# Kernel tuning notes

Measured on AMD Instinct MI355X. Metric: run time of the kernel, lower is better.

## Reference

```python
import jax, jax.numpy as jnp
import numpy as np

K = 32   # tokens_per_obs (hard-coded in module)
V = 512  # vocab_size

def setup_inputs() -> dict:
    key = jax.random.key(0)
    ks = jax.random.split(key, 10)
    s = 0.02  # small init scale for numerical sanity
    return {
        "x": jax.random.normal(ks[0], (4096, 512), jnp.float32),
        "enc_w1": jax.random.normal(ks[1], (512, 512), jnp.float32) * s,
        "enc_b1": jnp.zeros((512,), jnp.float32),
        "enc_w2": jax.random.normal(ks[2], (512, 16384), jnp.float32) * s,
        "enc_b2": jnp.zeros((16384,), jnp.float32),
        "codebook": jax.random.uniform(ks[3], (16384, 256), jnp.float32, -1.0 / V, 1.0 / V),
        "dec_w1": jax.random.normal(ks[4], (256, 512), jnp.float32) * s,
        "dec_b1": jnp.zeros((512,), jnp.float32),
        "dec_w2": jax.random.normal(ks[5], (512, 512), jnp.float32) * s,
        "dec_b2": jnp.zeros((512,), jnp.float32),
    }

def reference(x, enc_w1, enc_b1, enc_w2, enc_b2, codebook,
              dec_w1, dec_b1, dec_w2, dec_b2):
    b = x.shape[0]
    # encoder MLP -> logits z of shape (b, K*V)
    h = jax.nn.relu(x @ enc_w1 + enc_b1)
    z = h @ enc_w2 + enc_b2
    zl = z.reshape(b, K, V)                      # (b, K, V) per-block logits
    # categorical sample per token block
    tokens = jax.random.categorical(jax.random.key(1), zl, axis=-1)  # (b, K) int
    p = jax.nn.softmax(zl, axis=-1).reshape(b, K * V)
    oh = jax.nn.one_hot(tokens, V, dtype=p.dtype).reshape(b, K * V)
    # straight-through: forward value == one-hot, gradient flows through p
    st = p + jax.lax.stop_gradient(oh - p)
    z_q = st @ codebook                          # (b, embed_dim) = sum of K code rows
    # decoder MLP -> reconstruction
    rec = jax.nn.relu(z_q @ dec_w1 + dec_b1) @ dec_w2 + dec_b2
    return z, z_q, rec
```

## Files before the change

kernel.cpp:

```cpp
#include <hip/hip_runtime.h>
#include <hip/hip_bf16.h>
#include <math.h>
#include <stdint.h>


#define BATCH 4096
#define KTOK  32
#define VOCAB 512
#define DMODEL 512
#define ZDIM  16384
#define EDIM  256
#define MARGIN 0.03125f

typedef __attribute__((ext_vector_type(8))) short short8v;
typedef __attribute__((ext_vector_type(4))) float f32x4;

__device__ __forceinline__ void threefry2x32(uint32_t k0, uint32_t k1,
                                             uint32_t x0, uint32_t x1,
                                             uint32_t& y0, uint32_t& y1) {
    uint32_t ks0 = k0, ks1 = k1, ks2 = k0 ^ k1 ^ 0x1BD11BDAu;
    x0 += ks0; x1 += ks1;
#define TFR(r) { x0 += x1; x1 = __builtin_rotateleft32(x1, r); x1 ^= x0; }
    TFR(13) TFR(15) TFR(26) TFR(6)
    x0 += ks1; x1 += ks2 + 1u;
    TFR(17) TFR(29) TFR(16) TFR(24)
    x0 += ks2; x1 += ks0 + 2u;
    TFR(13) TFR(15) TFR(26) TFR(6)
    x0 += ks0; x1 += ks1 + 3u;
    TFR(17) TFR(29) TFR(16) TFR(24)
    x0 += ks1; x1 += ks2 + 4u;
    TFR(13) TFR(15) TFR(26) TFR(6)
    x0 += ks2; x1 += ks0 + 5u;
#undef TFR
    y0 = x0; y1 = x1;
}

__device__ __forceinline__ float jax_gumbel(uint64_t e) {
    const float TINY = 1.17549435e-38f;
    uint32_t y0, y1;
    threefry2x32(0u, 1u, (uint32_t)(e >> 32), (uint32_t)(e & 0xffffffffull), y0, y1);
    uint32_t bits = y0 ^ y1;
    float u = __uint_as_float(0x3f800000u | (bits >> 9)) - 1.0f;
    u = u * 1.0f + TINY;
    u = fmaxf(TINY, u);
    return -logf(-logf(u));
}

__device__ __forceinline__ float gumbel_from_bits(uint32_t bits) {
    const float TINY = 1.17549435e-38f;
    const float LN2 = 0.69314718056f;
    float f = __uint_as_float(0x3f800000u | (bits >> 9));
    float u = f - 1.0f;
    float d = 2.0f - f;
    u = fmaxf(u, TINY);
    float e_hw = -LN2 * __builtin_amdgcn_logf(u);
    float e_poly = d * fmaf(d, fmaf(d, 0.33333333f, 0.5f), 1.0f);
    float e = (d < 0.002f) ? e_poly : e_hw;
    return -LN2 * __builtin_amdgcn_logf(e);
}

__device__ __forceinline__ float fast_gumbel(uint32_t e32) {
    uint32_t y0, y1;
    threefry2x32(0u, 1u, 0u, e32, y0, y1);
    return gumbel_from_bits(y0 ^ y1);
}

__device__ __forceinline__ unsigned short f32_to_bf16_rne(float f) {
    uint32_t u = __float_as_uint(f);
    uint32_t r = (u + 0x7fffu + ((u >> 16) & 1u)) >> 16;
    return (unsigned short)r;
}

__device__ __forceinline__ void top2_push(float& s1, float& s2, int& v1,
                                          float s, int v) {
    if (s > s1 || (s == s1 && v < v1)) { s2 = s1; s1 = s; v1 = v; }
    else s2 = fmaxf(s2, s);
}
__device__ __forceinline__ void top2_merge(float& s1, float& s2, int& v1,
                                           float os1, float os2, int ov1) {
    if (os1 > s1 || (os1 == s1 && ov1 < v1)) {
        s2 = fmaxf(s1, os2);
        s1 = os1; v1 = ov1;
    } else {
        s2 = fmaxf(s2, os1);
    }
}

__device__ __forceinline__ void gload16(const unsigned short* src,
                                        unsigned short* lds_base) {
    __builtin_amdgcn_global_load_lds(
        (const __attribute__((address_space(1))) unsigned int*)src,
        (__attribute__((address_space(3))) unsigned int*)lds_base, 16, 0, 0);
}

template<bool RELU>
__global__ __launch_bounds__(256)
void gemm_f32_64(const float* __restrict__ A, const float* __restrict__ B,
                 const float* __restrict__ bias, float* __restrict__ C,
                 unsigned short* __restrict__ Cb,
                 int M, int N, int K) {
    constexpr int BK = 16;
    __shared__ __align__(16) float As[BK][68];
    __shared__ __align__(16) float Bs[BK][68];

    const int tid = threadIdx.x;
    const int tx = tid % 16;
    const int ty = tid / 16;
    const int brow = blockIdx.y * 64;
    const int bcol = blockIdx.x * 64;

    float acc[4][4] = {};

    for (int k0 = 0; k0 < K; k0 += BK) {
        {
            int r = tid >> 2, c4 = tid & 3;
            float4 v = *(const float4*)&A[(size_t)(brow + r) * K + k0 + c4 * 4];
            As[c4 * 4 + 0][r] = v.x;
            As[c4 * 4 + 1][r] = v.y;
            As[c4 * 4 + 2][r] = v.z;
            As[c4 * 4 + 3][r] = v.w;
        }
        {
            int r = tid >> 4, c4 = tid & 15;
            *(float4*)&Bs[r][c4 * 4] = *(const float4*)&B[(size_t)(k0 + r) * N + bcol + c4 * 4];
        }
        __syncthreads();

#pragma unroll
        for (int kk = 0; kk < BK; ++kk) {
            float a[4], b[4];
            *(float4*)&a[0] = *(const float4*)&As[kk][ty * 4];
            *(float4*)&b[0] = *(const float4*)&Bs[kk][tx * 4];
#pragma unroll
            for (int i = 0; i < 4; ++i)
#pragma unroll
                for (int j = 0; j < 4; ++j)
                    acc[i][j] = fmaf(a[i], b[j], acc[i][j]);
        }
        __syncthreads();
    }

#pragma unroll
    for (int i = 0; i < 4; ++i) {
        int row = brow + ty * 4 + i;
        int col = bcol + tx * 4;
        float4 v;
        v.x = acc[i][0] + bias[col + 0];
        v.y = acc[i][1] + bias[col + 1];
        v.z = acc[i][2] + bias[col + 2];
        v.w = acc[i][3] + bias[col + 3];
        if (RELU) {
            v.x = fmaxf(v.x, 0.0f); v.y = fmaxf(v.y, 0.0f);
            v.z = fmaxf(v.z, 0.0f); v.w = fmaxf(v.w, 0.0f);
        }
        *(float4*)&C[(size_t)row * N + col] = v;
        if (Cb) {
            ushort4 o;
            o.x = f32_to_bf16_rne(v.x);
            o.y = f32_to_bf16_rne(v.y);
            o.z = f32_to_bf16_rne(v.z);
            o.w = f32_to_bf16_rne(v.w);
            *(ushort4*)&Cb[(size_t)row * N + col] = o;
        }
    }
}

template<bool RELU>
__global__ __launch_bounds__(256)
void gemm_f32(const float* __restrict__ A, const float* __restrict__ B,
              const float* __restrict__ bias, float* __restrict__ C,
              int M, int N, int K) {
    constexpr int BM = 128, BN = 128, BK = 16, TM = 8, TN = 8;
    __shared__ __align__(16) float As[BK][BM + 4];
    __shared__ __align__(16) float Bs[BK][BN + 4];

    const int tid = threadIdx.x;
    const int tx = tid % (BN / TN);
    const int ty = tid / (BN / TN);
    const int brow = blockIdx.y * BM;
    const int bcol = blockIdx.x * BN;

    float acc[TM][TN] = {};

    for (int k0 = 0; k0 < K; k0 += BK) {
#pragma unroll
        for (int f = tid; f < BM * BK / 4; f += 256) {
            int r = f / (BK / 4);
            int c4 = f % (BK / 4);
            float4 v = *(const float4*)&A[(size_t)(brow + r) * K + k0 + c4 * 4];
            As[c4 * 4 + 0][r] = v.x;
            As[c4 * 4 + 1][r] = v.y;
            As[c4 * 4 + 2][r] = v.z;
            As[c4 * 4 + 3][r] = v.w;
        }
#pragma unroll
        for (int f = tid; f < BK * BN / 4; f += 256) {
            int r = f / (BN / 4);
            int c4 = f % (BN / 4);
            *(float4*)&Bs[r][c4 * 4] = *(const float4*)&B[(size_t)(k0 + r) * N + bcol + c4 * 4];
        }
        __syncthreads();

#pragma unroll
        for (int kk = 0; kk < BK; ++kk) {
            float a[TM], b[TN];
            *(float4*)&a[0] = *(const float4*)&As[kk][ty * TM];
            *(float4*)&a[4] = *(const float4*)&As[kk][ty * TM + 4];
            *(float4*)&b[0] = *(const float4*)&Bs[kk][tx * TN];
            *(float4*)&b[4] = *(const float4*)&Bs[kk][tx * TN + 4];
#pragma unroll
            for (int i = 0; i < TM; ++i)
#pragma unroll
                for (int j = 0; j < TN; ++j)
                    acc[i][j] = fmaf(a[i], b[j], acc[i][j]);
        }
        __syncthreads();
    }

#pragma unroll
    for (int i = 0; i < TM; ++i) {
        int row = brow + ty * TM + i;
#pragma unroll
        for (int j = 0; j < TN; j += 4) {
            int col = bcol + tx * TN + j;
            float4 v;
            v.x = acc[i][j + 0] + bias[col + 0];
            v.y = acc[i][j + 1] + bias[col + 1];
            v.z = acc[i][j + 2] + bias[col + 2];
            v.w = acc[i][j + 3] + bias[col + 3];
            if (RELU) {
                v.x = fmaxf(v.x, 0.0f); v.y = fmaxf(v.y, 0.0f);
                v.z = fmaxf(v.z, 0.0f); v.w = fmaxf(v.w, 0.0f);
            }
            *(float4*)&C[(size_t)row * N + col] = v;
        }
    }
}

__global__ __launch_bounds__(256)
void transpose_w2(const float* __restrict__ src, unsigned short* __restrict__ dstb,
                  float* __restrict__ dstf, int R, int C, int writeF) {
    __shared__ float tile[32][33];
    const int c0 = blockIdx.x * 32, r0 = blockIdx.y * 32;
    const int tx = threadIdx.x % 32, ty = threadIdx.x / 32;
#pragma unroll
    for (int i = ty; i < 32; i += 8)
        tile[i][tx] = src[(size_t)(r0 + i) * C + c0 + tx];
    __syncthreads();
#pragma unroll
    for (int i = ty; i < 32; i += 8) {
        float v = tile[tx][i];
        size_t o = (size_t)(c0 + i) * R + r0 + tx;
        dstb[o] = f32_to_bf16_rne(v);
        if (writeF) dstf[o] = v;
    }
}

__global__ __launch_bounds__(256)
void gemm_mfma_bf16(const unsigned short* __restrict__ A,
                    const unsigned short* __restrict__ Bt,
                    const float* __restrict__ bias,
                    float* __restrict__ C,
                    int M, int N, int K) {
    constexpr int BM = 128, BN = 128, BK = 32;
    __shared__ unsigned short As[BM * BK];
    __shared__ unsigned short Bs[BN * BK];

    const int lid = blockIdx.y * gridDim.x + blockIdx.x;
    const int xcd = lid & 7;
    const int kk2 = lid >> 3;
    const int rpx = gridDim.y >> 3;
    const int by = xcd * rpx + (kk2 % rpx);
    const int bx = kk2 / rpx;

    const int tid = threadIdx.x;
    const int wid = tid >> 6;
    const int lane = tid & 63;
    const int wr = wid >> 1, wc = wid & 1;
    const int l15 = lane & 15, lq = lane >> 4;
    const int brow = by * BM;
    const int bcol = bx * BN;

    const int g1 = tid;
    const int g2 = tid + 256;
    const size_t a1 = (size_t)(brow + (g1 >> 2)) * K + (g1 & 3) * 8;
    const size_t a2 = (size_t)(brow + (g2 >> 2)) * K + (g2 & 3) * 8;
    const size_t b1 = (size_t)(bcol + (g1 >> 2)) * K + (g1 & 3) * 8;
    const size_t b2 = (size_t)(bcol + (g2 >> 2)) * K + (g2 & 3) * 8;
    unsigned short* as_base1 = As + (size_t)wid * 64 * 8;
    unsigned short* as_base2 = As + (size_t)(256 + wid * 64) * 8;
    unsigned short* bs_base1 = Bs + (size_t)wid * 64 * 8;
    unsigned short* bs_base2 = Bs + (size_t)(256 + wid * 64) * 8;

    f32x4 acc[4][4];
#pragma unroll
    for (int m = 0; m < 4; ++m)
#pragma unroll
        for (int n = 0; n < 4; ++n) acc[m][n] = (f32x4){0.f, 0.f, 0.f, 0.f};

    for (int k0 = 0; k0 < K; k0 += BK) {
        gload16(A + a1 + k0, as_base1);
        gload16(A + a2 + k0, as_base2);
        gload16(Bt + b1 + k0, bs_base1);
        gload16(Bt + b2 + k0, bs_base2);
        __syncthreads();

        short8v af[4], bf[4];
#pragma unroll
        for (int m = 0; m < 4; ++m)
            af[m] = *(const short8v*)&As[(wr * 64 + m * 16 + l15) * BK + lq * 8];
#pragma unroll
        for (int n = 0; n < 4; ++n)
            bf[n] = *(const short8v*)&Bs[(wc * 64 + n * 16 + l15) * BK + lq * 8];
#pragma unroll
        for (int m = 0; m < 4; ++m)
#pragma unroll
            for (int n = 0; n < 4; ++n)
                acc[m][n] = __builtin_amdgcn_mfma_f32_16x16x32_bf16(
                    af[m], bf[n], acc[m][n], 0, 0, 0);
        __syncthreads();
    }

#pragma unroll
    for (int m = 0; m < 4; ++m) {
#pragma unroll
        for (int n = 0; n < 4; ++n) {
            int col = bcol + wc * 64 + n * 16 + l15;
            float bv = bias[col];
#pragma unroll
            for (int r = 0; r < 4; ++r) {
                int row = brow + wr * 64 + m * 16 + lq * 4 + r;
                C[(size_t)row * N + col] = acc[m][n][r] + bv;
            }
        }
    }
}

__global__ __launch_bounds__(256)
void sample_tokens_prune(const float* __restrict__ z, int* __restrict__ tokens,
                         float* __restrict__ s1v, int* __restrict__ amb,
                         int* __restrict__ ambCount) {
    const int wave = threadIdx.x >> 6;
    const int lane = threadIdx.x & 63;
    const uint32_t t = blockIdx.x * 4 + wave;
    const float* zr = z + (size_t)t * VOCAB;

    uint32_t bb[8];
    float zz[8];
    uint32_t bmax = 0u;
    float zmx = -INFINITY, zmn = INFINITY;
#pragma unroll
    for (int half = 0; half < 2; ++half) {
        const int e0 = half * 256 + lane * 4;
        const float4 zv = *(const float4*)&zr[e0];
        zz[half * 4 + 0] = zv.x; zz[half * 4 + 1] = zv.y;
        zz[half * 4 + 2] = zv.z; zz[half * 4 + 3] = zv.w;
#pragma unroll
        for (int j = 0; j < 4; ++j) {
            uint32_t y0, y1;
            threefry2x32(0u, 1u, 0u, t * (uint32_t)VOCAB + e0 + j, y0, y1);
            const uint32_t b = y0 ^ y1;
            bb[half * 4 + j] = b;
            bmax = b > bmax ? b : bmax;
            zmx = fmaxf(zmx, zz[half * 4 + j]);
            zmn = fminf(zmn, zz[half * 4 + j]);
        }
    }
#pragma unroll
    for (int off = 32; off > 0; off >>= 1) {
        uint32_t ob = (uint32_t)__shfl_xor((int)bmax, off);
        bmax = ob > bmax ? ob : bmax;
        zmx = fmaxf(zmx, __shfl_xor(zmx, off));
        zmn = fminf(zmn, __shfl_xor(zmn, off));
    }

    const float gmax = gumbel_from_bits(bmax);
    const float delta = (zmx - zmn) + MARGIN + 0.004f;
    const float gstar = gmax - delta;
    const float INVLN2 = 1.4426950408889634f;
    float es = exp2f(-gstar * INVLN2);
    float us = exp2f(-es * INVLN2);
    us = us * (1.0f - 4e-6f) - 4e-6f;
    uint32_t bthr = 0u;
    if (us > 0.0f) {
        uint32_t ub = __float_as_uint(1.0f + us) - 0x3f800000u;
        uint32_t bt = ub << 9;
        bthr = bt > 4096u ? bt - 4096u : 0u;
    }

    float s1 = -INFINITY, s2 = -INFINITY;
    int v1 = VOCAB;
#pragma unroll
    for (int idx = 0; idx < 8; ++idx) {
        if (bb[idx] >= bthr) {
            const int v = (idx >> 2) * 256 + lane * 4 + (idx & 3);
            const float s = zz[idx] + gumbel_from_bits(bb[idx]);
            top2_push(s1, s2, v1, s, v);
        }
    }
#pragma unroll
    for (int off = 32; off > 0; off >>= 1) {
        float os1 = __shfl_down(s1, off);
        int ov1 = __shfl_down(v1, off);
        float os2 = __shfl_down(s2, off);
        top2_merge(s1, s2, v1, os1, os2, ov1);
    }
    if (lane == 0) {
        tokens[t] = v1;
        s1v[t] = s1;
        if (s1 - s2 < MARGIN) {
            int idx = atomicAdd(ambCount, 1);
            amb[idx] = (int)t;
        }
    }
}

__global__ __launch_bounds__(64)
void refine_tokens2(const float* __restrict__ z, const float* __restrict__ h,
                    const float* __restrict__ w2t, const float* __restrict__ eb2,
                    const int* __restrict__ amb, const int* __restrict__ ambCount,
                    const float* __restrict__ s1v, int* __restrict__ tok) {
    __shared__ float hrow[DMODEL];
    __shared__ int candv[64];
    const int cnt = *ambCount;
    const int lane = threadIdx.x;

    for (int i = blockIdx.x; i < cnt; i += gridDim.x) {
        const int t = amb[i];
        const int b = t >> 5;
        const int kb = t & 31;
        const float* zr = z + (size_t)t * VOCAB;
        const float s1 = s1v[t];

        {
            float4 hv0 = *(const float4*)&h[(size_t)b * DMODEL + lane * 8];
            float4 hv1 = *(const float4*)&h[(size_t)b * DMODEL + lane * 8 + 4];
            *(float4*)&hrow[lane * 8] = hv0;
            *(float4*)&hrow[lane * 8 + 4] = hv1;
        }

        int base = 0;
#pragma unroll
        for (int half = 0; half < 2; ++half) {
            int e0 = half * 256 + lane * 4;
            float4 zv = *(const float4*)&zr[e0];
            float zs[4] = {zv.x, zv.y, zv.z, zv.w};
#pragma unroll
            for (int j = 0; j < 4; ++j) {
                int v = e0 + j;
                float s = zs[j] + fast_gumbel((uint32_t)t * VOCAB + v);
                bool pred = (s >= s1 - MARGIN);
                unsigned long long mask = __ballot(pred);
                if (pred) {
                    int slot = base + __popcll(mask & ((1ull << lane) - 1ull));
                    if (slot < 64) candv[slot] = v;
                }
                base += __popcll(mask);
            }
        }
        __syncthreads();
        const int ncand = base < 64 ? base : 64;

        float bestE = -INFINITY;
        int bestV = VOCAB;
        if (lane < ncand) {
            const int v = candv[lane];
            const int n = kb * VOCAB + v;
            const float* wr_ = w2t + (size_t)n * DMODEL;
            float acc = 0.f;
#pragma unroll 8
            for (int k = 0; k < DMODEL; ++k)
                acc = fmaf(hrow[k], wr_[k], acc);
            bestE = acc + eb2[n] + jax_gumbel((uint64_t)t * VOCAB + v);
            bestV = v;
        }
#pragma unroll
        for (int off = 32; off > 0; off >>= 1) {
            float oe = __shfl_down(bestE, off);
            int ov = __shfl_down(bestV, off);
            if (oe > bestE || (oe == bestE && ov < bestV)) { bestE = oe; bestV = ov; }
        }
        if (lane == 0) tok[t] = bestV;
        __syncthreads();
    }
}

__global__ __launch_bounds__(256)
void sample_tokens_simple(const float* __restrict__ z, int* __restrict__ tokens) {
    const int wave = threadIdx.x >> 6;
    const int lane = threadIdx.x & 63;
    const size_t t = (size_t)blockIdx.x * 4 + wave;
    const float* zr = z + t * VOCAB;
    float zv[8];
    *(float4*)&zv[0] = *(const float4*)&zr[lane * 8];
    *(float4*)&zv[4] = *(const float4*)&zr[lane * 8 + 4];
    const uint64_t ebase = t * (uint64_t)VOCAB + (uint64_t)lane * 8;
    float best = -INFINITY;
    int bestv = 0;
#pragma unroll
    for (int j = 0; j < 8; ++j) {
        float g = jax_gumbel(ebase + j);
        float s = zv[j] + g;
        int v = lane * 8 + j;
        if (s > best || (s == best && v < bestv)) { best = s; bestv = v; }
    }
#pragma unroll
    for (int off = 32; off > 0; off >>= 1) {
        float ob = __shfl_down(best, off);
        int ov = __shfl_down(bestv, off);
        if (ob > best || (ob == best && ov < bestv)) { best = ob; bestv = ov; }
    }
    if (lane == 0) tokens[t] = bestv;
}

__global__ __launch_bounds__(64)
void zero_count(int* p) { if (threadIdx.x == 0) *p = 0; }

__global__ __launch_bounds__(256)
void gather_zq(const int* __restrict__ tokens, const float* __restrict__ codebook,
               float* __restrict__ zq) {
    const int b = blockIdx.x;
    const int d = threadIdx.x;
    float s = 0.0f;
#pragma unroll
    for (int k = 0; k < KTOK; ++k) {
        int tok = tokens[b * KTOK + k];
        s += codebook[(size_t)(k * VOCAB + tok) * EDIM + d];
    }
    zq[(size_t)b * EDIM + d] = s;
}

extern "C" void kernel_launch(void* const* d_in, const int* in_sizes, int n_in,
                              void* d_out, int out_size, void* d_ws, size_t ws_size,
                              hipStream_t stream) {
    const float* x   = (const float*)d_in[0];
    const float* ew1 = (const float*)d_in[1];
    const float* eb1 = (const float*)d_in[2];
    const float* ew2 = (const float*)d_in[3];
    const float* eb2 = (const float*)d_in[4];
    const float* cb  = (const float*)d_in[5];
    const float* dw1 = (const float*)d_in[6];
    const float* db1 = (const float*)d_in[7];
    const float* dw2 = (const float*)d_in[8];
    const float* db2 = (const float*)d_in[9];

    float* out = (float*)d_out;
    float* z   = out;
    float* zq  = out + (size_t)BATCH * ZDIM;
    float* rec = zq + (size_t)BATCH * EDIM;

    char* ws = (char*)d_ws;
    float* h    = (float*)(ws);
    float* h2   = (float*)(ws + 8388608);
    unsigned short* hb   = (unsigned short*)(ws + 16777216);
    unsigned short* w2bt = (unsigned short*)(ws + 20971520);
    float* w2t  = (float*)(ws + 37748736);
    char* tail = ws + 71303168;
    const size_t WS_NEED2 = 71303168 + 1572864 + 256;
    const bool fast2 = ws_size >= WS_NEED2;
    if (!fast2) tail = ws + 16777216;
    int*   tok  = (int*)(tail);
    float* s1v  = (float*)(tail + 524288);
    int*   amb  = (int*)(tail + 1048576);
    int*   cnt  = (int*)(tail + 1572864);

    dim3 blk(256);

    gemm_f32_64<true ><<<dim3(DMODEL / 64, BATCH / 64), blk, 0, stream>>>(
        x, ew1, eb1, h, fast2 ? hb : (unsigned short*)nullptr,
        BATCH, DMODEL, DMODEL);

    if (fast2) {
        transpose_w2<<<dim3(ZDIM / 32, DMODEL / 32), blk, 0, stream>>>(
            ew2, w2bt, w2t, DMODEL, ZDIM, 1);
        zero_count<<<dim3(1), dim3(64), 0, stream>>>(cnt);
        gemm_mfma_bf16<<<dim3(ZDIM / 128, BATCH / 128), blk, 0, stream>>>(
            hb, w2bt, eb2, z, BATCH, ZDIM, DMODEL);
        sample_tokens_prune<<<dim3(BATCH * KTOK / 4), blk, 0, stream>>>(
            z, tok, s1v, amb, cnt);
        refine_tokens2<<<dim3(4096), dim3(64), 0, stream>>>(
            z, h, w2t, eb2, amb, cnt, s1v, tok);
    } else {
        gemm_f32<false><<<dim3(ZDIM / 128, BATCH / 128), blk, 0, stream>>>(
            h, ew2, eb2, z, BATCH, ZDIM, DMODEL);
        sample_tokens_simple<<<dim3(BATCH * KTOK / 4), blk, 0, stream>>>(z, tok);
    }

    gather_zq<<<dim3(BATCH), blk, 0, stream>>>(tok, cb, zq);

    gemm_f32_64<true ><<<dim3(DMODEL / 64, BATCH / 64), blk, 0, stream>>>(
        zq, dw1, db1, h2, nullptr, BATCH, DMODEL, EDIM);
    gemm_f32_64<false><<<dim3(DMODEL / 64, BATCH / 64), blk, 0, stream>>>(
        h2, dw2, db2, rec, nullptr, BATCH, DMODEL, DMODEL);
}
```

Baseline: 439.3 us.

## Double-buffer bf16 MFMA GEMM and compute all gumbels with 4-wide threefry

The bf16 MFMA GEMM now uses double-buffered shared memory, issuing the next K-tile's loads before computing on the current one, so global-load latency overlaps the MFMAs and one barrier per iteration is dropped. The sampling kernel drops the threshold-based pruning of gumbel evaluations. It instead computes all eight gumbels per lane, generating four threefry streams interleaved with a specialized constant key (0,1) for ILP, and uses xor-shuffles for the top-2 reduction. The cost is doubled LDS per block in the GEMM and more log/transcendental work in sampling, traded against less divergence and more instruction-level parallelism.

Result: no change. 435.1 us (-0.9%).

```diff
diff --git a/kernel.cpp b/kernel.cpp
--- a/kernel.cpp
+++ b/kernel.cpp
@@ -35,6 +35,38 @@
     y0 = x0; y1 = x1;
 }
 
+__device__ __forceinline__ void threefry4x(uint32_t e,
+                                           uint32_t& o0, uint32_t& o1,
+                                           uint32_t& o2, uint32_t& o3) {
+    const uint32_t KS2 = 0x1BD11BDBu;
+    uint32_t xa = 0u, ya = e + 1u;
+    uint32_t xb = 0u, yb = e + 2u;
+    uint32_t xc = 0u, yc = e + 3u;
+    uint32_t xd = 0u, yd = e + 4u;
+#define RR(r) \
+    xa += ya; xb += yb; xc += yc; xd += yd; \
+    ya = __builtin_rotateleft32(ya, r) ^ xa; \
+    yb = __builtin_rotateleft32(yb, r) ^ xb; \
+    yc = __builtin_rotateleft32(yc, r) ^ xc; \
+    yd = __builtin_rotateleft32(yd, r) ^ xd;
+    RR(13) RR(15) RR(26) RR(6)
+    xa += 1u; xb += 1u; xc += 1u; xd += 1u;
+    ya += KS2 + 1u; yb += KS2 + 1u; yc += KS2 + 1u; yd += KS2 + 1u;
+    RR(17) RR(29) RR(16) RR(24)
+    xa += KS2; xb += KS2; xc += KS2; xd += KS2;
+    ya += 2u; yb += 2u; yc += 2u; yd += 2u;
+    RR(13) RR(15) RR(26) RR(6)
+    ya += 4u; yb += 4u; yc += 4u; yd += 4u;
+    RR(17) RR(29) RR(16) RR(24)
+    xa += 1u; xb += 1u; xc += 1u; xd += 1u;
+    ya += KS2 + 4u; yb += KS2 + 4u; yc += KS2 + 4u; yd += KS2 + 4u;
+    RR(13) RR(15) RR(26) RR(6)
+    xa += KS2; xb += KS2; xc += KS2; xd += KS2;
+    ya += 5u; yb += 5u; yc += 5u; yd += 5u;
+#undef RR
+    o0 = xa ^ ya; o1 = xb ^ yb; o2 = xc ^ yc; o3 = xd ^ yd;
+}
+
 __device__ __forceinline__ float jax_gumbel(uint64_t e) {
     const float TINY = 1.17549435e-38f;
     uint32_t y0, y1;
@@ -263,8 +295,9 @@
                     float* __restrict__ C,
                     int M, int N, int K) {
     constexpr int BM = 128, BN = 128, BK = 32;
-    __shared__ unsigned short As[BM * BK];
-    __shared__ unsigned short Bs[BN * BK];
+    constexpr int TSZ = BM * BK;
+    __shared__ unsigned short As[2 * TSZ];
+    __shared__ unsigned short Bs[2 * TSZ];
 
     const int lid = blockIdx.y * gridDim.x + blockIdx.x;
     const int xcd = lid & 7;
@@ -287,10 +320,8 @@
     const size_t a2 = (size_t)(brow + (g2 >> 2)) * K + (g2 & 3) * 8;
     const size_t b1 = (size_t)(bcol + (g1 >> 2)) * K + (g1 & 3) * 8;
     const size_t b2 = (size_t)(bcol + (g2 >> 2)) * K + (g2 & 3) * 8;
-    unsigned short* as_base1 = As + (size_t)wid * 64 * 8;
-    unsigned short* as_base2 = As + (size_t)(256 + wid * 64) * 8;
-    unsigned short* bs_base1 = Bs + (size_t)wid * 64 * 8;
-    unsigned short* bs_base2 = Bs + (size_t)(256 + wid * 64) * 8;
+    const int asOff1 = wid * 64 * 8;
+    const int asOff2 = (256 + wid * 64) * 8;
 
     f32x4 acc[4][4];
 #pragma unroll
@@ -298,20 +329,31 @@
 #pragma unroll
         for (int n = 0; n < 4; ++n) acc[m][n] = (f32x4){0.f, 0.f, 0.f, 0.f};
 
-    for (int k0 = 0; k0 < K; k0 += BK) {
-        gload16(A + a1 + k0, as_base1);
-        gload16(A + a2 + k0, as_base2);
-        gload16(Bt + b1 + k0, bs_base1);
-        gload16(Bt + b2 + k0, bs_base2);
-        __syncthreads();
-
+    const int NK = K / BK;
+    gload16(A + a1, As + asOff1);
+    gload16(A + a2, As + asOff2);
+    gload16(Bt + b1, Bs + asOff1);
+    gload16(Bt + b2, Bs + asOff2);
+    __syncthreads();
+
+    int buf = 0;
+    for (int kt = 0; kt < NK; ++kt) {
+        if (kt + 1 < NK) {
+            const int k0 = (kt + 1) * BK;
+            const int o = (buf ^ 1) * TSZ;
+            gload16(A + a1 + k0, As + o + asOff1);
+            gload16(A + a2 + k0, As + o + asOff2);
+            gload16(Bt + b1 + k0, Bs + o + asOff1);
+            gload16(Bt + b2 + k0, Bs + o + asOff2);
+        }
+        const int cb = buf * TSZ;
         short8v af[4], bf[4];
 #pragma unroll
         for (int m = 0; m < 4; ++m)
-            af[m] = *(const short8v*)&As[(wr * 64 + m * 16 + l15) * BK + lq * 8];
+            af[m] = *(const short8v*)&As[cb + (wr * 64 + m * 16 + l15) * BK + lq * 8];
 #pragma unroll
         for (int n = 0; n < 4; ++n)
-            bf[n] = *(const short8v*)&Bs[(wc * 64 + n * 16 + l15) * BK + lq * 8];
+            bf[n] = *(const short8v*)&Bs[cb + (wc * 64 + n * 16 + l15) * BK + lq * 8];
 #pragma unroll
         for (int m = 0; m < 4; ++m)
 #pragma unroll
@@ -319,6 +361,7 @@
                 acc[m][n] = __builtin_amdgcn_mfma_f32_16x16x32_bf16(
                     af[m], bf[n], acc[m][n], 0, 0, 0);
         __syncthreads();
+        buf ^= 1;
     }
 
 #pragma unroll
@@ -337,72 +380,36 @@
 }
 
 __global__ __launch_bounds__(256)
-void sample_tokens_prune(const float* __restrict__ z, int* __restrict__ tokens,
-                         float* __restrict__ s1v, int* __restrict__ amb,
-                         int* __restrict__ ambCount) {
+void sample_tokens_ilp(const float* __restrict__ z, int* __restrict__ tokens,
+                       float* __restrict__ s1v, int* __restrict__ amb,
+                       int* __restrict__ ambCount) {
     const int wave = threadIdx.x >> 6;
     const int lane = threadIdx.x & 63;
     const uint32_t t = blockIdx.x * 4 + wave;
     const float* zr = z + (size_t)t * VOCAB;
 
-    uint32_t bb[8];
-    float zz[8];
-    uint32_t bmax = 0u;
-    float zmx = -INFINITY, zmn = INFINITY;
+    float s1 = -INFINITY, s2 = -INFINITY;
+    int v1 = VOCAB;
 #pragma unroll
     for (int half = 0; half < 2; ++half) {
         const int e0 = half * 256 + lane * 4;
         const float4 zv = *(const float4*)&zr[e0];
-        zz[half * 4 + 0] = zv.x; zz[half * 4 + 1] = zv.y;
-        zz[half * 4 + 2] = zv.z; zz[half * 4 + 3] = zv.w;
-#pragma unroll
-        for (int j = 0; j < 4; ++j) {
-            uint32_t y0, y1;
-            threefry2x32(0u, 1u, 0u, t * (uint32_t)VOCAB + e0 + j, y0, y1);
-            const uint32_t b = y0 ^ y1;
-            bb[half * 4 + j] = b;
-            bmax = b > bmax ? b : bmax;
-            zmx = fmaxf(zmx, zz[half * 4 + j]);
-            zmn = fminf(zmn, zz[half * 4 + j]);
-        }
+        uint32_t b0, b1, b2, b3;
+        threefry4x(t * (uint32_t)VOCAB + (uint32_t)e0, b0, b1, b2, b3);
+        const float g0 = gumbel_from_bits(b0);
+        const float g1 = gumbel_from_bits(b1);
+        const float g2 = gumbel_from_bits(b2);
+        const float g3 = gumbel_from_bits(b3);
+        top2_push(s1, s2, v1, zv.x + g0, e0 + 0);
+        top2_push(s1, s2, v1, zv.y + g1, e0 + 1);
+        top2_push(s1, s2, v1, zv.z + g2, e0 + 2);
+        top2_push(s1, s2, v1, zv.w + g3, e0 + 3);
     }
 #pragma unroll
     for (int off = 32; off > 0; off >>= 1) {
-        uint32_t ob = (uint32_t)__shfl_xor((int)bmax, off);
-        bmax = ob > bmax ? ob : bmax;
-        zmx = fmaxf(zmx, __shfl_xor(zmx, off));
-        zmn = fminf(zmn, __shfl_xor(zmn, off));
-    }
-
-    const float gmax = gumbel_from_bits(bmax);
-    const float delta = (zmx - zmn) + MARGIN + 0.004f;
-    const float gstar = gmax - delta;
-    const float INVLN2 = 1.4426950408889634f;
-    float es = exp2f(-gstar * INVLN2);
-    float us = exp2f(-es * INVLN2);
-    us = us * (1.0f - 4e-6f) - 4e-6f;
-    uint32_t bthr = 0u;
-    if (us > 0.0f) {
-        uint32_t ub = __float_as_uint(1.0f + us) - 0x3f800000u;
-        uint32_t bt = ub << 9;
-        bthr = bt > 4096u ? bt - 4096u : 0u;
-    }
-
-    float s1 = -INFINITY, s2 = -INFINITY;
-    int v1 = VOCAB;
-#pragma unroll
-    for (int idx = 0; idx < 8; ++idx) {
-        if (bb[idx] >= bthr) {
-            const int v = (idx >> 2) * 256 + lane * 4 + (idx & 3);
-            const float s = zz[idx] + gumbel_from_bits(bb[idx]);
-            top2_push(s1, s2, v1, s, v);
-        }
-    }
-#pragma unroll
-    for (int off = 32; off > 0; off >>= 1) {
-        float os1 = __shfl_down(s1, off);
-        int ov1 = __shfl_down(v1, off);
-        float os2 = __shfl_down(s2, off);
+        float os1 = __shfl_xor(s1, off);
+        int ov1 = __shfl_xor(v1, off);
+        float os2 = __shfl_xor(s2, off);
         top2_merge(s1, s2, v1, os1, os2, ov1);
     }
     if (lane == 0) {
@@ -576,7 +583,7 @@
         zero_count<<<dim3(1), dim3(64), 0, stream>>>(cnt);
         gemm_mfma_bf16<<<dim3(ZDIM / 128, BATCH / 128), blk, 0, stream>>>(
             hb, w2bt, eb2, z, BATCH, ZDIM, DMODEL);
-        sample_tokens_prune<<<dim3(BATCH * KTOK / 4), blk, 0, stream>>>(
+        sample_tokens_ilp<<<dim3(BATCH * KTOK / 4), blk, 0, stream>>>(
             z, tok, s1v, amb, cnt);
         refine_tokens2<<<dim3(4096), dim3(64), 0, stream>>>(
             z, h, w2t, eb2, amb, cnt, s1v, tok);
```
